# Performance work log

Hardware: AMD Instinct MI355X
Metric: run time of the kernel (lower is better)

Reference implementation:

```python
import jax, jax.numpy as jnp
import numpy as np

D, H, W = 128, 128, 128
MAX_R = 2  # static; equals min(ceil(max radius_vox), 20) given scales <= 0.01 -> radius <= 1.92
N_PTS = 100000


def quaternion_to_rotation_matrix(q):
    # q: (N, 4) as (w, x, y, z)
    q = q / jnp.linalg.norm(q, axis=-1, keepdims=True)
    w, x, y, z = q[..., 0], q[..., 1], q[..., 2], q[..., 3]
    r00 = 1 - 2 * (y * y + z * z); r01 = 2 * (x * y - w * z); r02 = 2 * (x * z + w * y)
    r10 = 2 * (x * y + w * z); r11 = 1 - 2 * (x * x + z * z); r12 = 2 * (y * z - w * x)
    r20 = 2 * (x * z - w * y); r21 = 2 * (y * z + w * x); r22 = 1 - 2 * (x * x + y * y)
    return jnp.stack([r00, r01, r02, r10, r11, r12, r20, r21, r22], axis=-1).reshape(q.shape[0], 3, 3)


def setup_inputs() -> dict:
    key = jax.random.key(0)
    k1, k2, k3, k4 = jax.random.split(key, 4)
    positions = jax.random.uniform(k1, (N_PTS, 3), minval=-1.0, maxval=1.0, dtype=jnp.float32)
    scales = jax.random.uniform(k2, (N_PTS, 3), minval=0.002, maxval=0.01, dtype=jnp.float32)
    rotations = jax.random.normal(k3, (N_PTS, 4), dtype=jnp.float32)
    density = jax.random.normal(k4, (N_PTS,), dtype=jnp.float32)
    return {"positions": positions, "scales": scales, "rotations": rotations,
            "density": density, "chunk_size": 4096}


def reference(positions, scales, rotations, density, chunk_size):
    # chunk_size only affects torch memory staging, not the math (single logical chunk here)
    shape_t = jnp.array([D, H, W], dtype=jnp.float32)
    center = (positions + 1.0) * 0.5 * shape_t - 0.5            # (N,3) voxel-space centers
    Rm = quaternion_to_rotation_matrix(rotations)                # (N,3,3)
    S_inv = 1.0 / (scales + 1e-8)                                # (N,3)
    L = Rm * S_inv[:, None, :]                                   # scale columns, as in torch R * S_inv.unsqueeze(1)
    cov_inv = jnp.einsum('nij,nkj->nik', L, L)                   # L @ L^T, (N,3,3)

    k_rng = jnp.arange(-MAX_R, MAX_R + 1)
    kz, ky, kx = jnp.meshgrid(k_rng, k_rng, k_rng, indexing='ij')
    offsets = jnp.stack([kz, ky, kx], axis=-1).reshape(-1, 3).astype(jnp.float32)  # (K,3), K=(2r+1)^3

    gc = jnp.round(center)[:, None, :] + offsets[None, :, :]     # (N,K,3) global voxel coords
    gz, gy, gx = gc[..., 0], gc[..., 1], gc[..., 2]
    valid = (gz >= 0) & (gz < D) & (gy >= 0) & (gy < H) & (gx >= 0) & (gx < W)

    diff_norm = (gc - center[:, None, :]) / (shape_t * 0.5)      # (N,K,3)
    mahal = jnp.einsum('nkd,nde,nke->nk', diff_norm, cov_inv, diff_norm)  # (N,K)
    mask = valid & (mahal <= 9.0)

    vals = jnp.where(mask, jnp.exp(-0.5 * mahal), 0.0) * density[:, None]  # (N,K)
    flat_idx = (gz.astype(jnp.int32) * (H * W) + gy.astype(jnp.int32) * W + gx.astype(jnp.int32))
    flat_idx = jnp.where(mask, flat_idx, 0)                      # masked entries carry zero value

    volume = jnp.zeros(D * H * W, dtype=jnp.float32).at[flat_idx.reshape(-1)].add(vals.reshape(-1))
    return volume.reshape(D, H, W)
```

## Files before the change

### kernel.cpp

```cpp
#include <hip/hip_runtime.h>


#define VOX_D 128
#define VOX_H 128
#define VOX_W 128
#define MAX_R 2

__global__ __launch_bounds__(256) void voxelize_splat(
    const float* __restrict__ positions,
    const float* __restrict__ scales,
    const float* __restrict__ rotations,
    const float* __restrict__ density,
    float* __restrict__ volume,
    int n)
{
    int i = blockIdx.x * blockDim.x + threadIdx.x;
    if (i >= n) return;

    const float p0 = positions[3 * i + 0];
    const float p1 = positions[3 * i + 1];
    const float p2 = positions[3 * i + 2];

    const float c0 = (p0 + 1.0f) * 64.0f - 0.5f;
    const float c1 = (p1 + 1.0f) * 64.0f - 0.5f;
    const float c2 = (p2 + 1.0f) * 64.0f - 0.5f;

    float qw = rotations[4 * i + 0];
    float qx = rotations[4 * i + 1];
    float qy = rotations[4 * i + 2];
    float qz = rotations[4 * i + 3];
    const float qn = rsqrtf(qw * qw + qx * qx + qy * qy + qz * qz);
    qw *= qn; qx *= qn; qy *= qn; qz *= qn;

    const float r00 = 1.0f - 2.0f * (qy * qy + qz * qz);
    const float r01 = 2.0f * (qx * qy - qw * qz);
    const float r02 = 2.0f * (qx * qz + qw * qy);
    const float r10 = 2.0f * (qx * qy + qw * qz);
    const float r11 = 1.0f - 2.0f * (qx * qx + qz * qz);
    const float r12 = 2.0f * (qy * qz - qw * qx);
    const float r20 = 2.0f * (qx * qz - qw * qy);
    const float r21 = 2.0f * (qy * qz + qw * qx);
    const float r22 = 1.0f - 2.0f * (qx * qx + qy * qy);

    const float si0 = 1.0f / (scales[3 * i + 0] + 1e-8f);
    const float si1 = 1.0f / (scales[3 * i + 1] + 1e-8f);
    const float si2 = 1.0f / (scales[3 * i + 2] + 1e-8f);

    const float dens = density[i];

    const int b0 = (int)rintf(c0);
    const int b1 = (int)rintf(c1);
    const int b2 = (int)rintf(c2);

    const float inv_half = 1.0f / 64.0f;

    float d0v[2 * MAX_R + 1], d1v[2 * MAX_R + 1], d2v[2 * MAX_R + 1];
    bool v0v[2 * MAX_R + 1], v1v[2 * MAX_R + 1], v2v[2 * MAX_R + 1];
#pragma unroll
    for (int k = -MAX_R; k <= MAX_R; ++k) {
        const int t = k + MAX_R;
        d0v[t] = ((float)(b0 + k) - c0) * inv_half;
        d1v[t] = ((float)(b1 + k) - c1) * inv_half;
        d2v[t] = ((float)(b2 + k) - c2) * inv_half;
        v0v[t] = (b0 + k >= 0) && (b0 + k < VOX_D);
        v1v[t] = (b1 + k >= 0) && (b1 + k < VOX_H);
        v2v[t] = (b2 + k >= 0) && (b2 + k < VOX_W);
    }

#pragma unroll
    for (int t0 = 0; t0 < 2 * MAX_R + 1; ++t0) {
        const float d0 = d0v[t0];
        const float a0 = r00 * d0;
        const float a1 = r01 * d0;
        const float a2 = r02 * d0;
        const int g0 = b0 + t0 - MAX_R;
#pragma unroll
        for (int t1 = 0; t1 < 2 * MAX_R + 1; ++t1) {
            const float d1 = d1v[t1];
            const float e0 = a0 + r10 * d1;
            const float e1 = a1 + r11 * d1;
            const float e2 = a2 + r12 * d1;
            const int g1 = b1 + t1 - MAX_R;
            const bool v01 = v0v[t0] && v1v[t1];
            const int base_idx = g0 * (VOX_H * VOX_W) + g1 * VOX_W;
#pragma unroll
            for (int t2 = 0; t2 < 2 * MAX_R + 1; ++t2) {
                const float d2 = d2v[t2];
                const float m0 = si0 * (e0 + r20 * d2);
                const float m1 = si1 * (e1 + r21 * d2);
                const float m2 = si2 * (e2 + r22 * d2);
                const float mahal = m0 * m0 + m1 * m1 + m2 * m2;
                const bool ok = v01 && v2v[t2] && (mahal <= 9.0f);
                if (ok) {
                    const float val = __expf(-0.5f * mahal) * dens;
                    atomicAdd(&volume[base_idx + (b2 + t2 - MAX_R)], val);
                }
            }
        }
    }
}

extern "C" void kernel_launch(void* const* d_in, const int* in_sizes, int n_in,
                              void* d_out, int out_size, void* d_ws, size_t ws_size,
                              hipStream_t stream) {
    const float* positions = (const float*)d_in[0];
    const float* scales    = (const float*)d_in[1];
    const float* rotations = (const float*)d_in[2];
    const float* density   = (const float*)d_in[3];
    float* volume = (float*)d_out;

    const int n = in_sizes[0] / 3;

    hipMemsetAsync(volume, 0, (size_t)out_size * sizeof(float), stream);

    const int block = 256;
    const int grid = (n + block - 1) / block;
    voxelize_splat<<<grid, block, 0, stream>>>(positions, scales, rotations,
                                               density, volume, n);
}
```

Baseline: 103.5 us.

## Split each Gaussian across five threads, one per z-offset plane

Each point is now handled by five threads instead of one, each thread covering a single z-plane of the 5x5x5 stencil. The aim is to expose more parallelism and shorten each thread's serial chain of atomics and math, which helps latency hiding with 100k points. In exchange, every thread redundantly loads the point's inputs and recomputes the quaternion rotation and inverse scales, and the grid launches five times as many threads.

```diff
diff --git a/kernel.cpp b/kernel.cpp
--- a/kernel.cpp
+++ b/kernel.cpp
@@ -5,6 +5,7 @@
 #define VOX_H 128
 #define VOX_W 128
 #define MAX_R 2
+#define KW (2 * MAX_R + 1)
 
 __global__ __launch_bounds__(256) void voxelize_splat(
     const float* __restrict__ positions,
@@ -14,8 +15,10 @@
     float* __restrict__ volume,
     int n)
 {
-    int i = blockIdx.x * blockDim.x + threadIdx.x;
-    if (i >= n) return;
+    const int tid = blockIdx.x * blockDim.x + threadIdx.x;
+    if (tid >= n * KW) return;
+    const int i  = tid / KW;
+    const int t0 = tid - i * KW;
 
     const float p0 = positions[3 * i + 0];
     const float p1 = positions[3 * i + 1];
@@ -24,6 +27,13 @@
     const float c0 = (p0 + 1.0f) * 64.0f - 0.5f;
     const float c1 = (p1 + 1.0f) * 64.0f - 0.5f;
     const float c2 = (p2 + 1.0f) * 64.0f - 0.5f;
+
+    const int b0 = (int)rintf(c0);
+    const int b1 = (int)rintf(c1);
+    const int b2 = (int)rintf(c2);
+
+    const int g0 = b0 + t0 - MAX_R;
+    if (g0 < 0 || g0 >= VOX_D) return;
 
     float qw = rotations[4 * i + 0];
     float qx = rotations[4 * i + 1];
@@ -47,54 +57,46 @@
     const float si2 = 1.0f / (scales[3 * i + 2] + 1e-8f);
 
     const float dens = density[i];
-
-    const int b0 = (int)rintf(c0);
-    const int b1 = (int)rintf(c1);
-    const int b2 = (int)rintf(c2);
-
     const float inv_half = 1.0f / 64.0f;
 
-    float d0v[2 * MAX_R + 1], d1v[2 * MAX_R + 1], d2v[2 * MAX_R + 1];
-    bool v0v[2 * MAX_R + 1], v1v[2 * MAX_R + 1], v2v[2 * MAX_R + 1];
+    const float d0 = ((float)g0 - c0) * inv_half;
+    const float a0 = r00 * d0;
+    const float a1 = r01 * d0;
+    const float a2 = r02 * d0;
+
+    float d1v[KW], d2v[KW];
+    bool v1v[KW], v2v[KW];
 #pragma unroll
     for (int k = -MAX_R; k <= MAX_R; ++k) {
         const int t = k + MAX_R;
-        d0v[t] = ((float)(b0 + k) - c0) * inv_half;
         d1v[t] = ((float)(b1 + k) - c1) * inv_half;
         d2v[t] = ((float)(b2 + k) - c2) * inv_half;
-        v0v[t] = (b0 + k >= 0) && (b0 + k < VOX_D);
         v1v[t] = (b1 + k >= 0) && (b1 + k < VOX_H);
         v2v[t] = (b2 + k >= 0) && (b2 + k < VOX_W);
     }
 
+    const int plane_base = g0 * (VOX_H * VOX_W);
+
 #pragma unroll
-    for (int t0 = 0; t0 < 2 * MAX_R + 1; ++t0) {
-        const float d0 = d0v[t0];
-        const float a0 = r00 * d0;
-        const float a1 = r01 * d0;
-        const float a2 = r02 * d0;
-        const int g0 = b0 + t0 - MAX_R;
+    for (int t1 = 0; t1 < KW; ++t1) {
+        const float d1 = d1v[t1];
+        const float e0 = a0 + r10 * d1;
+        const float e1 = a1 + r11 * d1;
+        const float e2 = a2 + r12 * d1;
+        const int g1 = b1 + t1 - MAX_R;
+        const bool v1 = v1v[t1];
+        const int row_base = plane_base + g1 * VOX_W;
 #pragma unroll
-        for (int t1 = 0; t1 < 2 * MAX_R + 1; ++t1) {
-            const float d1 = d1v[t1];
-            const float e0 = a0 + r10 * d1;
-            const float e1 = a1 + r11 * d1;
-            const float e2 = a2 + r12 * d1;
-            const int g1 = b1 + t1 - MAX_R;
-            const bool v01 = v0v[t0] && v1v[t1];
-            const int base_idx = g0 * (VOX_H * VOX_W) + g1 * VOX_W;
-#pragma unroll
-            for (int t2 = 0; t2 < 2 * MAX_R + 1; ++t2) {
-                const float d2 = d2v[t2];
-                const float m0 = si0 * (e0 + r20 * d2);
-                const float m1 = si1 * (e1 + r21 * d2);
-                const float m2 = si2 * (e2 + r22 * d2);
-                const float mahal = m0 * m0 + m1 * m1 + m2 * m2;
-                const bool ok = v01 && v2v[t2] && (mahal <= 9.0f);
-                if (ok) {
-                    const float val = __expf(-0.5f * mahal) * dens;
-                    atomicAdd(&volume[base_idx + (b2 + t2 - MAX_R)], val);
-                }
+        for (int t2 = 0; t2 < KW; ++t2) {
+            const float d2 = d2v[t2];
+            const float m0 = si0 * (e0 + r20 * d2);
+            const float m1 = si1 * (e1 + r21 * d2);
+            const float m2 = si2 * (e2 + r22 * d2);
+            const float mahal = m0 * m0 + m1 * m1 + m2 * m2;
+            const bool ok = v1 && v2v[t2] && (mahal <= 9.0f);
+            if (ok) {
+                const float val = __expf(-0.5f * mahal) * dens;
+                atomicAdd(&volume[row_base + (b2 + t2 - MAX_R)], val);
             }
         }
     }
@@ -114,7 +116,8 @@
     hipMemsetAsync(volume, 0, (size_t)out_size * sizeof(float), stream);
 
     const int block = 256;
-    const int grid = (n + block - 1) / block;
+    const int total = n * KW;
+    const int grid = (total + block - 1) / block;
     voxelize_splat<<<grid, block, 0, stream>>>(positions, scales, rotations,
                                                density, volume, n);
 }
```

After: 99.94 us. -3.4%, faster.

## Replace global atomic scatter with per-tile shared-memory gather after a prep pass

Applied to the files above, without the earlier changes.

Adds a prep kernel that computes voxel centers, packed base coordinates and the scaled rotation rows per point once. A second kernel assigns each block an 8x16x32 voxel tile. The block scans every point, queues the ones that overlap the tile, accumulates their contributions with shared-memory atomics, and writes the finished tile with coalesced float4 stores. This removes the global memset and the global atomics. In exchange, every one of the 512 blocks scans all N points, and a tile with more than CAP hits falls back to serial per-thread splatting. Points whose rounded center lies outside 0..255 may also be misencoded by the 8-bit packing, though the test inputs stay inside the grid.

```diff
diff --git a/kernel.cpp b/kernel.cpp
--- a/kernel.cpp
+++ b/kernel.cpp
@@ -1,29 +1,32 @@
 #include <hip/hip_runtime.h>
 
 
-#define VOX_D 128
-#define VOX_H 128
-#define VOX_W 128
-#define MAX_R 2
+#define VOX 128
+#define W0 8
+#define W1 16
+#define W2 32
+#define CAP 2048
 
-__global__ __launch_bounds__(256) void voxelize_splat(
+__global__ __launch_bounds__(256) void prep_points(
     const float* __restrict__ positions,
     const float* __restrict__ scales,
     const float* __restrict__ rotations,
     const float* __restrict__ density,
-    float* __restrict__ volume,
+    unsigned int* __restrict__ packed,
+    float4* __restrict__ rec,
     int n)
 {
-    int i = blockIdx.x * blockDim.x + threadIdx.x;
+    const int i = blockIdx.x * blockDim.x + threadIdx.x;
     if (i >= n) return;
 
-    const float p0 = positions[3 * i + 0];
-    const float p1 = positions[3 * i + 1];
-    const float p2 = positions[3 * i + 2];
+    const float c0 = (positions[3 * i + 0] + 1.0f) * 64.0f - 0.5f;
+    const float c1 = (positions[3 * i + 1] + 1.0f) * 64.0f - 0.5f;
+    const float c2 = (positions[3 * i + 2] + 1.0f) * 64.0f - 0.5f;
 
-    const float c0 = (p0 + 1.0f) * 64.0f - 0.5f;
-    const float c1 = (p1 + 1.0f) * 64.0f - 0.5f;
-    const float c2 = (p2 + 1.0f) * 64.0f - 0.5f;
+    const int b0 = (int)rintf(c0);
+    const int b1 = (int)rintf(c1);
+    const int b2 = (int)rintf(c2);
+    packed[i] = (unsigned)b0 | ((unsigned)b1 << 8) | ((unsigned)b2 << 16);
 
     float qw = rotations[4 * i + 0];
     float qx = rotations[4 * i + 1];
@@ -46,57 +49,110 @@
     const float si1 = 1.0f / (scales[3 * i + 1] + 1e-8f);
     const float si2 = 1.0f / (scales[3 * i + 2] + 1e-8f);
 
-    const float dens = density[i];
+    rec[4 * i + 0] = make_float4(c0, c1, c2, density[i]);
+    rec[4 * i + 1] = make_float4(si0 * r00, si0 * r10, si0 * r20, 0.0f);
+    rec[4 * i + 2] = make_float4(si1 * r01, si1 * r11, si1 * r21, 0.0f);
+    rec[4 * i + 3] = make_float4(si2 * r02, si2 * r12, si2 * r22, 0.0f);
+}
 
-    const int b0 = (int)rintf(c0);
-    const int b1 = (int)rintf(c1);
-    const int b2 = (int)rintf(c2);
+__device__ __forceinline__ void splat_site(
+    float* tile, int k, int b0, int b1, int b2, int X0, int X1, int X2,
+    const float4& r0, const float4& r1, const float4& r2, const float4& r3)
+{
+    const int dz = k / 25;
+    const int rm = k - dz * 25;
+    const int dy = rm / 5;
+    const int dx = rm - dy * 5;
+    const int g0 = b0 + dz - 2;
+    const int g1 = b1 + dy - 2;
+    const int g2 = b2 + dx - 2;
+    const int l0 = g0 - X0;
+    const int l1 = g1 - X1;
+    const int l2 = g2 - X2;
+    if ((unsigned)l0 < W0 && (unsigned)l1 < W1 && (unsigned)l2 < W2) {
+        const float d0 = ((float)g0 - r0.x) * (1.0f / 64.0f);
+        const float d1 = ((float)g1 - r0.y) * (1.0f / 64.0f);
+        const float d2 = ((float)g2 - r0.z) * (1.0f / 64.0f);
+        const float m0 = r1.x * d0 + r1.y * d1 + r1.z * d2;
+        const float m1 = r2.x * d0 + r2.y * d1 + r2.z * d2;
+        const float m2 = r3.x * d0 + r3.y * d1 + r3.z * d2;
+        const float mah = m0 * m0 + m1 * m1 + m2 * m2;
+        if (mah <= 9.0f) {
+            atomicAdd(&tile[(l0 * W1 + l1) * W2 + l2], __expf(-0.5f * mah) * r0.w);
+        }
+    }
+}
 
-    const float inv_half = 1.0f / 64.0f;
+__global__ __launch_bounds__(256) void voxelize_tiles(
+    const unsigned int* __restrict__ packed,
+    const float4* __restrict__ rec,
+    float* __restrict__ volume,
+    int n)
+{
+    __shared__ float tile[W0 * W1 * W2];
+    __shared__ int queue[CAP];
+    __shared__ int qn;
 
-    float d0v[2 * MAX_R + 1], d1v[2 * MAX_R + 1], d2v[2 * MAX_R + 1];
-    bool v0v[2 * MAX_R + 1], v1v[2 * MAX_R + 1], v2v[2 * MAX_R + 1];
-#pragma unroll
-    for (int k = -MAX_R; k <= MAX_R; ++k) {
-        const int t = k + MAX_R;
-        d0v[t] = ((float)(b0 + k) - c0) * inv_half;
-        d1v[t] = ((float)(b1 + k) - c1) * inv_half;
-        d2v[t] = ((float)(b2 + k) - c2) * inv_half;
-        v0v[t] = (b0 + k >= 0) && (b0 + k < VOX_D);
-        v1v[t] = (b1 + k >= 0) && (b1 + k < VOX_H);
-        v2v[t] = (b2 + k >= 0) && (b2 + k < VOX_W);
-    }
+    const int t = threadIdx.x;
+    const int X2 = blockIdx.x * W2;
+    const int X1 = blockIdx.y * W1;
+    const int X0 = blockIdx.z * W0;
 
-#pragma unroll
-    for (int t0 = 0; t0 < 2 * MAX_R + 1; ++t0) {
-        const float d0 = d0v[t0];
-        const float a0 = r00 * d0;
-        const float a1 = r01 * d0;
-        const float a2 = r02 * d0;
-        const int g0 = b0 + t0 - MAX_R;
-#pragma unroll
-        for (int t1 = 0; t1 < 2 * MAX_R + 1; ++t1) {
-            const float d1 = d1v[t1];
-            const float e0 = a0 + r10 * d1;
-            const float e1 = a1 + r11 * d1;
-            const float e2 = a2 + r12 * d1;
-            const int g1 = b1 + t1 - MAX_R;
-            const bool v01 = v0v[t0] && v1v[t1];
-            const int base_idx = g0 * (VOX_H * VOX_W) + g1 * VOX_W;
-#pragma unroll
-            for (int t2 = 0; t2 < 2 * MAX_R + 1; ++t2) {
-                const float d2 = d2v[t2];
-                const float m0 = si0 * (e0 + r20 * d2);
-                const float m1 = si1 * (e1 + r21 * d2);
-                const float m2 = si2 * (e2 + r22 * d2);
-                const float mahal = m0 * m0 + m1 * m1 + m2 * m2;
-                const bool ok = v01 && v2v[t2] && (mahal <= 9.0f);
-                if (ok) {
-                    const float val = __expf(-0.5f * mahal) * dens;
-                    atomicAdd(&volume[base_idx + (b2 + t2 - MAX_R)], val);
-                }
+    for (int v = t; v < W0 * W1 * W2; v += 256) tile[v] = 0.0f;
+    if (t == 0) qn = 0;
+    __syncthreads();
+
+#pragma unroll 4
+    for (int p = t; p < n; p += 256) {
+        const unsigned u = packed[p];
+        const int b0 = u & 255;
+        const int b1 = (u >> 8) & 255;
+        const int b2 = (u >> 16) & 255;
+        const bool hit = (b0 >= X0 - 2) & (b0 <= X0 + W0 + 1) &
+                         (b1 >= X1 - 2) & (b1 <= X1 + W1 + 1) &
+                         (b2 >= X2 - 2) & (b2 <= X2 + W2 + 1);
+        if (hit) {
+            const int slot = atomicAdd(&qn, 1);
+            if (slot < CAP) {
+                queue[slot] = p;
+            } else {
+                const float4 r0 = rec[4 * p + 0];
+                const float4 r1 = rec[4 * p + 1];
+                const float4 r2 = rec[4 * p + 2];
+                const float4 r3 = rec[4 * p + 3];
+                for (int k = 0; k < 125; ++k)
+                    splat_site(tile, k, b0, b1, b2, X0, X1, X2, r0, r1, r2, r3);
             }
         }
+    }
+    __syncthreads();
+    int nq = qn; if (nq > CAP) nq = CAP;
+
+    const int half = t >> 7;
+    const int k = t & 127;
+    for (int j = half; j < nq; j += 2) {
+        const int p = queue[j];
+        const float4 r0 = rec[4 * p + 0];
+        const float4 r1 = rec[4 * p + 1];
+        const float4 r2 = rec[4 * p + 2];
+        const float4 r3 = rec[4 * p + 3];
+        const unsigned u = packed[p];
+        const int b0 = u & 255;
+        const int b1 = (u >> 8) & 255;
+        const int b2 = (u >> 16) & 255;
+        if (k < 125)
+            splat_site(tile, k, b0, b1, b2, X0, X1, X2, r0, r1, r2, r3);
+    }
+    __syncthreads();
+
+    const float4* tl4 = (const float4*)tile;
+    for (int cid = t; cid < (W0 * W1 * W2) / 4; cid += 256) {
+        const int l2q = cid & (W2 / 4 - 1);
+        const int row = cid >> 3;
+        const int l1 = row & (W1 - 1);
+        const int l0 = row >> 4;
+        const int gelem = ((X0 + l0) * VOX + (X1 + l1)) * VOX + X2 + l2q * 4;
+        ((float4*)volume)[gelem >> 2] = tl4[cid];
     }
 }
 
@@ -111,10 +167,12 @@
 
     const int n = in_sizes[0] / 3;
 
-    hipMemsetAsync(volume, 0, (size_t)out_size * sizeof(float), stream);
+    unsigned int* packed = (unsigned int*)d_ws;
+    float4* rec = (float4*)((char*)d_ws + (1 << 20));
 
-    const int block = 256;
-    const int grid = (n + block - 1) / block;
-    voxelize_splat<<<grid, block, 0, stream>>>(positions, scales, rotations,
-                                               density, volume, n);
+    prep_points<<<(n + 255) / 256, 256, 0, stream>>>(
+        positions, scales, rotations, density, packed, rec, n);
+
+    dim3 grid(VOX / W2, VOX / W1, VOX / W0);
+    voxelize_tiles<<<grid, 256, 0, stream>>>(packed, rec, volume, n);
 }
```

Result: slower. 322.6 us (+211.8%).

## Bin Gaussians into volume tiles and splat via shared-memory atomics

Applied to the files above, without the earlier changes.

Splits the work into two kernels. The first computes each Gaussian's center, density and scaled rotation rows into a packed per-point record, then appends the point index to every 4x8x32 tile its 5x5x5 footprint touches. The second kernel runs one block per tile: it accumulates contributions with shared-memory atomics and writes the finished tile to the volume with float4 stores, so the separate volume memset is no longer needed. This replaces millions of contended global atomics with LDS atomics. The costs are the extra binning pass and record traffic, poor thread use when a tile holds few points, and silently dropped points if any tile exceeds its fixed capacity of 1024.

```diff
diff --git a/kernel.cpp b/kernel.cpp
--- a/kernel.cpp
+++ b/kernel.cpp
@@ -1,29 +1,33 @@
 #include <hip/hip_runtime.h>
 
 
-#define VOX_D 128
-#define VOX_H 128
-#define VOX_W 128
-#define MAX_R 2
+#define VOX 128
+#define T0 4
+#define T1 8
+#define T2 32
+#define NT0 (VOX / T0)
+#define NT1 (VOX / T1)
+#define NT2 (VOX / T2)
+#define NCELL (NT0 * NT1 * NT2)
+#define CAP 1024
 
-__global__ __launch_bounds__(256) void voxelize_splat(
+
+__global__ __launch_bounds__(256) void bin_points(
     const float* __restrict__ positions,
     const float* __restrict__ scales,
     const float* __restrict__ rotations,
     const float* __restrict__ density,
-    float* __restrict__ volume,
+    unsigned int* __restrict__ counts,
+    int* __restrict__ bins,
+    float4* __restrict__ rec,
     int n)
 {
-    int i = blockIdx.x * blockDim.x + threadIdx.x;
+    const int i = blockIdx.x * blockDim.x + threadIdx.x;
     if (i >= n) return;
 
-    const float p0 = positions[3 * i + 0];
-    const float p1 = positions[3 * i + 1];
-    const float p2 = positions[3 * i + 2];
-
-    const float c0 = (p0 + 1.0f) * 64.0f - 0.5f;
-    const float c1 = (p1 + 1.0f) * 64.0f - 0.5f;
-    const float c2 = (p2 + 1.0f) * 64.0f - 0.5f;
+    const float c0 = (positions[3 * i + 0] + 1.0f) * 64.0f - 0.5f;
+    const float c1 = (positions[3 * i + 1] + 1.0f) * 64.0f - 0.5f;
+    const float c2 = (positions[3 * i + 2] + 1.0f) * 64.0f - 0.5f;
 
     float qw = rotations[4 * i + 0];
     float qx = rotations[4 * i + 1];
@@ -46,58 +50,98 @@
     const float si1 = 1.0f / (scales[3 * i + 1] + 1e-8f);
     const float si2 = 1.0f / (scales[3 * i + 2] + 1e-8f);
 
-    const float dens = density[i];
+    rec[4 * i + 0] = make_float4(c0, c1, c2, density[i]);
+    rec[4 * i + 1] = make_float4(si0 * r00, si0 * r10, si0 * r20, 0.0f);
+    rec[4 * i + 2] = make_float4(si1 * r01, si1 * r11, si1 * r21, 0.0f);
+    rec[4 * i + 3] = make_float4(si2 * r02, si2 * r12, si2 * r22, 0.0f);
 
     const int b0 = (int)rintf(c0);
     const int b1 = (int)rintf(c1);
     const int b2 = (int)rintf(c2);
 
-    const float inv_half = 1.0f / 64.0f;
+    const int z_lo = max(b0 - 2, 0) / T0, z_hi = min(b0 + 2, VOX - 1) / T0;
+    const int y_lo = max(b1 - 2, 0) / T1, y_hi = min(b1 + 2, VOX - 1) / T1;
+    const int x_lo = max(b2 - 2, 0) / T2, x_hi = min(b2 + 2, VOX - 1) / T2;
 
-    float d0v[2 * MAX_R + 1], d1v[2 * MAX_R + 1], d2v[2 * MAX_R + 1];
-    bool v0v[2 * MAX_R + 1], v1v[2 * MAX_R + 1], v2v[2 * MAX_R + 1];
-#pragma unroll
-    for (int k = -MAX_R; k <= MAX_R; ++k) {
-        const int t = k + MAX_R;
-        d0v[t] = ((float)(b0 + k) - c0) * inv_half;
-        d1v[t] = ((float)(b1 + k) - c1) * inv_half;
-        d2v[t] = ((float)(b2 + k) - c2) * inv_half;
-        v0v[t] = (b0 + k >= 0) && (b0 + k < VOX_D);
-        v1v[t] = (b1 + k >= 0) && (b1 + k < VOX_H);
-        v2v[t] = (b2 + k >= 0) && (b2 + k < VOX_W);
-    }
+    for (int tz = z_lo; tz <= z_hi; ++tz)
+        for (int ty = y_lo; ty <= y_hi; ++ty)
+            for (int tx = x_lo; tx <= x_hi; ++tx) {
+                const int cell = (tz * NT1 + ty) * NT2 + tx;
+                const unsigned slot = atomicAdd(&counts[cell], 1u);
+                if (slot < CAP) bins[cell * CAP + slot] = i;
+            }
+}
 
-#pragma unroll
-    for (int t0 = 0; t0 < 2 * MAX_R + 1; ++t0) {
-        const float d0 = d0v[t0];
-        const float a0 = r00 * d0;
-        const float a1 = r01 * d0;
-        const float a2 = r02 * d0;
-        const int g0 = b0 + t0 - MAX_R;
-#pragma unroll
-        for (int t1 = 0; t1 < 2 * MAX_R + 1; ++t1) {
-            const float d1 = d1v[t1];
-            const float e0 = a0 + r10 * d1;
-            const float e1 = a1 + r11 * d1;
-            const float e2 = a2 + r12 * d1;
-            const int g1 = b1 + t1 - MAX_R;
-            const bool v01 = v0v[t0] && v1v[t1];
-            const int base_idx = g0 * (VOX_H * VOX_W) + g1 * VOX_W;
-#pragma unroll
-            for (int t2 = 0; t2 < 2 * MAX_R + 1; ++t2) {
-                const float d2 = d2v[t2];
-                const float m0 = si0 * (e0 + r20 * d2);
-                const float m1 = si1 * (e1 + r21 * d2);
-                const float m2 = si2 * (e2 + r22 * d2);
-                const float mahal = m0 * m0 + m1 * m1 + m2 * m2;
-                const bool ok = v01 && v2v[t2] && (mahal <= 9.0f);
-                if (ok) {
-                    const float val = __expf(-0.5f * mahal) * dens;
-                    atomicAdd(&volume[base_idx + (b2 + t2 - MAX_R)], val);
+__global__ __launch_bounds__(256) void splat_tiles(
+    const unsigned int* __restrict__ counts,
+    const int* __restrict__ bins,
+    const float4* __restrict__ rec,
+    float* __restrict__ volume)
+{
+    __shared__ float tile[T0 * T1 * T2];
+
+    const int t = threadIdx.x;
+    const int tx = blockIdx.x, ty = blockIdx.y, tz = blockIdx.z;
+    const int X0 = tz * T0, X1 = ty * T1, X2 = tx * T2;
+    const int cell = (tz * NT1 + ty) * NT2 + tx;
+
+    for (int v = t; v < T0 * T1 * T2; v += 256) tile[v] = 0.0f;
+    __syncthreads();
+
+    int nq = (int)counts[cell];
+    if (nq > CAP) nq = CAP;
+
+    for (int j = t; j < nq; j += 256) {
+        const int p = bins[cell * CAP + j];
+        const float4 r0 = rec[4 * p + 0];
+        const float4 r1 = rec[4 * p + 1];
+        const float4 r2 = rec[4 * p + 2];
+        const float4 r3 = rec[4 * p + 3];
+
+        const int b0 = (int)rintf(r0.x);
+        const int b1 = (int)rintf(r0.y);
+        const int b2 = (int)rintf(r0.z);
+
+        const int lo0 = max(b0 - 2, X0), hi0 = min(b0 + 2, X0 + T0 - 1);
+        const int lo1 = max(b1 - 2, X1), hi1 = min(b1 + 2, X1 + T1 - 1);
+        const int lo2 = max(b2 - 2, X2), hi2 = min(b2 + 2, X2 + T2 - 1);
+
+        const float inv_half = 1.0f / 64.0f;
+        for (int g0 = lo0; g0 <= hi0; ++g0) {
+            const float d0 = ((float)g0 - r0.x) * inv_half;
+            const float f0 = r1.x * d0;
+            const float f1 = r2.x * d0;
+            const float f2 = r3.x * d0;
+            const int base0 = (g0 - X0) * T1;
+            for (int g1 = lo1; g1 <= hi1; ++g1) {
+                const float d1 = ((float)g1 - r0.y) * inv_half;
+                const float e0 = f0 + r1.y * d1;
+                const float e1 = f1 + r2.y * d1;
+                const float e2 = f2 + r3.y * d1;
+                const int base1 = (base0 + (g1 - X1)) * T2;
+                for (int g2 = lo2; g2 <= hi2; ++g2) {
+                    const float d2 = ((float)g2 - r0.z) * inv_half;
+                    const float m0 = e0 + r1.z * d2;
+                    const float m1 = e1 + r2.z * d2;
+                    const float m2 = e2 + r3.z * d2;
+                    const float mah = m0 * m0 + m1 * m1 + m2 * m2;
+                    if (mah <= 9.0f) {
+                        atomicAdd(&tile[base1 + (g2 - X2)],
+                                  __expf(-0.5f * mah) * r0.w);
+                    }
                 }
             }
         }
     }
+    __syncthreads();
+
+    const float4* tl4 = (const float4*)tile;
+    const int row = t >> 3;
+    const int ch  = t & 7;
+    const int l0 = row >> 3;
+    const int l1 = row & 7;
+    const int g = ((X0 + l0) * VOX + (X1 + l1)) * VOX + X2 + ch * 4;
+    ((float4*)volume)[g >> 2] = tl4[t];
 }
 
 extern "C" void kernel_launch(void* const* d_in, const int* in_sizes, int n_in,
@@ -111,10 +155,15 @@
 
     const int n = in_sizes[0] / 3;
 
-    hipMemsetAsync(volume, 0, (size_t)out_size * sizeof(float), stream);
+    unsigned int* counts = (unsigned int*)d_ws;
+    int* bins            = (int*)((char*)d_ws + (1 << 20));
+    float4* rec          = (float4*)((char*)d_ws + (16 << 20));
 
-    const int block = 256;
-    const int grid = (n + block - 1) / block;
-    voxelize_splat<<<grid, block, 0, stream>>>(positions, scales, rotations,
-                                               density, volume, n);
+    hipMemsetAsync(counts, 0, NCELL * sizeof(unsigned int), stream);
+
+    bin_points<<<(n + 255) / 256, 256, 0, stream>>>(
+        positions, scales, rotations, density, counts, bins, rec, n);
+
+    dim3 grid(NT2, NT1, NT0);
+    splat_tiles<<<grid, 256, 0, stream>>>(counts, bins, rec, volume);
 }
```

Measured after the change: 135.7 us. +31.1%, slower.
